# Kernel tuning notes

Measured on AMD Instinct MI355X. Metric: run time of the kernel, lower is better.

Reference implementation:

```python
import jax, jax.numpy as jnp
import numpy as np

N = 100000   # nodes
F = 128      # feature dim (== numEdges ctor arg)
H = 64       # hidden_dim
E = 1600000  # edges (avg degree 16)


def setup_inputs() -> dict:
    key = jax.random.key(0)
    ks = jax.random.split(key, 8)
    x = jax.random.normal(ks[0], (N, F), dtype=jnp.float32)
    edge_index = jax.random.randint(ks[1], (2, E), 0, N)
    sF = 1.0 / np.sqrt(F)
    sH = 1.0 / np.sqrt(H)
    conv_W = jax.random.normal(ks[2], (F, F), dtype=jnp.float32) * sF  # GCNConv linear weight
    conv_b = jnp.zeros((F,), dtype=jnp.float32)
    w1 = jax.random.normal(ks[3], (H, F), dtype=jnp.float32) * sF
    b1 = jnp.zeros((H,), dtype=jnp.float32)
    w2 = jax.random.normal(ks[4], (H, H), dtype=jnp.float32) * sH
    b2 = jnp.zeros((H,), dtype=jnp.float32)
    w3 = jax.random.normal(ks[5], (1, H), dtype=jnp.float32) * sH
    b3 = jnp.zeros((1,), dtype=jnp.float32)
    return dict(x=x, edge_index=edge_index, conv_W=conv_W, conv_b=conv_b,
                w1=w1, b1=b1, w2=w2, b2=b2, w3=w3, b3=b3)


def reference(x, edge_index, conv_W, conv_b, w1, b1, w2, b2, w3, b3):
    n = x.shape[0]
    # --- GCNConv: D^{-1/2}(A+I)D^{-1/2} X W + b ---
    xw = x @ conv_W.T                                   # [N, F]
    loops = jnp.arange(n)
    src = jnp.concatenate([edge_index[0], loops])       # add self-loops
    dst = jnp.concatenate([edge_index[1], loops])
    deg = jax.ops.segment_sum(jnp.ones(src.shape[0], xw.dtype), dst, num_segments=n)
    dinv = jnp.where(deg > 0, jax.lax.rsqrt(deg), 0.0)
    norm = dinv[src] * dinv[dst]                        # [E+N]
    h = jax.ops.segment_sum(xw[src] * norm[:, None], dst, num_segments=n) + conv_b  # [N, F]
    # --- MedianAggregation (index=None -> single segment, 'lower' interpolation) ---
    med = jnp.sort(h, axis=0)[(n - 1) // 2][None, :]    # [1, F]
    # --- tanh MLP ---
    a = jnp.tanh(med @ w1.T + b1)
    a = jnp.tanh(a @ w2.T + b2)
    return a @ w3.T + b3                                # [1, 1]
```

## Files before the change

### kernel.cpp

```cpp
#include <hip/hip_runtime.h>
#include <math.h>


#define CAP    24576
#define CCAP   96
#define CSTR   97
#define DSTR   32
#define OVCAP  4096
#define SPCAP  2048
#define BCAP   4608
#define NBKMAX 400
#define CH     4096

typedef __attribute__((ext_vector_type(8))) short short8;
typedef __attribute__((ext_vector_type(4))) float f32x4;
typedef __attribute__((ext_vector_type(8))) _Float16 half8;
typedef __attribute__((ext_vector_type(2))) _Float16 half2v;

__device__ __forceinline__ unsigned ordKey(float x) {
    unsigned u = __float_as_uint(x);
    return (u & 0x80000000u) ? ~u : (u | 0x80000000u);
}
__device__ __forceinline__ unsigned short f2bf(float f) {
    unsigned u = __float_as_uint(f);
    return (unsigned short)((u + 0x7FFFu + ((u >> 16) & 1u)) >> 16);
}

__global__ void k_init(int* __restrict__ cursor, int* __restrict__ below,
                       int* __restrict__ candCnt, int* __restrict__ ovCnt,
                       const float* __restrict__ W, short* __restrict__ Whi,
                       short* __restrict__ Wlo, int nbk) {
    if (blockIdx.x == 1) {
        for (int idx = threadIdx.x; idx < 16384; idx += 256) {
            int j = idx & 7, lane = (idx >> 3) & 63;
            int t = (idx >> 9) & 7, s = idx >> 12;
            int row = t * 16 + (lane & 15);
            int k = s * 32 + (lane >> 4) * 8 + j;
            float w = W[row * 128 + k];
            unsigned short hb = f2bf(w);
            float hf = __uint_as_float((unsigned)hb << 16);
            Whi[idx] = (short)hb;
            Wlo[idx] = (short)f2bf(w - hf);
        }
        return;
    }
    int t = threadIdx.x;
    for (int i = t; i < nbk; i += 256) cursor[i] = 0;
    if (t < 128) { below[t] = 0; candCnt[t] = 0; }
    if (t == 0) { ovCnt[0] = 0; ovCnt[1] = 0; ovCnt[2] = 0; }
}

__global__ __launch_bounds__(256) void k_gemm(
        const float* __restrict__ x, const short* __restrict__ Whi,
        const short* __restrict__ Wlo, _Float16* __restrict__ xw, int n) {
    __shared__ float trn[4 * 16 * 132];
    const int t = threadIdx.x;
    const int lane = t & 63, wv = t >> 6;
    const int quad = lane >> 4, m = lane & 15;
    const int rowBase = blockIdx.x * 64 + wv * 16;
    const int r = rowBase + m;
    const int rl = r < n ? r : (n - 1);
    f32x4 acc[8];
    #pragma unroll
    for (int q = 0; q < 8; q++) acc[q] = (f32x4){0.f, 0.f, 0.f, 0.f};
    #pragma unroll
    for (int s = 0; s < 4; s++) {
        const float* xp = x + (size_t)rl * 128 + s * 32 + quad * 8;
        float4 p0 = *(const float4*)xp;
        float4 p1 = *(const float4*)(xp + 4);
        float f[8] = {p0.x, p0.y, p0.z, p0.w, p1.x, p1.y, p1.z, p1.w};
        short8 ah, al;
        #pragma unroll
        for (int j = 0; j < 8; j++) {
            unsigned short hb = f2bf(f[j]);
            float hf = __uint_as_float((unsigned)hb << 16);
            ah[j] = (short)hb;
            al[j] = (short)f2bf(f[j] - hf);
        }
        #pragma unroll
        for (int q = 0; q < 8; q++) {
            short8 bh = *(const short8*)(Whi + (((s * 8 + q) * 64 + lane) << 3));
            short8 bl = *(const short8*)(Wlo + (((s * 8 + q) * 64 + lane) << 3));
            acc[q] = __builtin_amdgcn_mfma_f32_16x16x32_bf16(ah, bh, acc[q], 0, 0, 0);
            acc[q] = __builtin_amdgcn_mfma_f32_16x16x32_bf16(al, bh, acc[q], 0, 0, 0);
            acc[q] = __builtin_amdgcn_mfma_f32_16x16x32_bf16(ah, bl, acc[q], 0, 0, 0);
        }
    }
    float* tw = trn + wv * (16 * 132);
    #pragma unroll
    for (int q = 0; q < 8; q++)
        #pragma unroll
        for (int e = 0; e < 4; e++)
            tw[(quad * 4 + e) * 132 + q * 16 + m] = acc[q][e];
    #pragma unroll
    for (int i = 0; i < 4; i++) {
        int row = i * 4 + (lane >> 4);
        int c8 = lane & 15;
        const float* tp = tw + row * 132 + c8 * 8;
        float4 p0 = *(const float4*)tp;
        float4 p1 = *(const float4*)(tp + 4);
        half8 o;
        o[0] = (_Float16)p0.x; o[1] = (_Float16)p0.y;
        o[2] = (_Float16)p0.z; o[3] = (_Float16)p0.w;
        o[4] = (_Float16)p1.x; o[5] = (_Float16)p1.y;
        o[6] = (_Float16)p1.z; o[7] = (_Float16)p1.w;
        int grow = rowBase + row;
        if (grow < n) *(half8*)(xw + (size_t)grow * 128 + c8 * 8) = o;
    }
}

__global__ __launch_bounds__(256) void k_bin(
        const int* __restrict__ src, const int* __restrict__ dst, int E,
        int* __restrict__ cursor, int2* __restrict__ binned,
        int* __restrict__ ovCnt, int2* __restrict__ ovBuf, int nbk) {
    __shared__ char smem[39168];
    const int t = threadIdx.x;
    int2* stage = (int2*)smem;
    int* hist  = (int*)(smem + 32768);
    int* gbase = hist + NBKMAX;
    int* hist2 = gbase + NBKMAX;
    int* sbase = hist2 + NBKMAX;
    const int e0 = (int)blockIdx.x * CH;
    const int len = min(CH, E - e0);
    for (int i = t; i < nbk; i += 256) { hist[i] = 0; hist2[i] = 0; }
    __syncthreads();
    for (int k = t; k < len; k += 256) {
        int s = src[e0 + k], d = dst[e0 + k];
        stage[k] = make_int2(s, d);
        atomicAdd(&hist[d >> 8], 1);
    }
    __syncthreads();
    for (int i = t; i < nbk; i += 256) {
        int c = hist[i];
        if (c) {
            int g = atomicAdd(&cursor[i], c);
            if (g + c <= BCAP) gbase[i] = g;
            else {
                gbase[i] = -1;
                sbase[i] = atomicAdd(ovCnt, c);
            }
        }
    }
    __syncthreads();
    for (int k = t; k < len; k += 256) {
        int2 e = stage[k];
        int b = e.y >> 8;
        int p = atomicAdd(&hist2[b], 1);
        int g = gbase[b];
        if (g >= 0) binned[(size_t)b * BCAP + g + p] = e;
        else {
            int o = sbase[b] + p;
            if (o < OVCAP) ovBuf[o] = make_int2(e.y, e.x);
        }
    }
}

__global__ __launch_bounds__(512) void k_build(int2* __restrict__ binned,
                                               const int* __restrict__ cursor,
                                               float* __restrict__ dinv,
                                               unsigned char* __restrict__ deg8,
                                               int* __restrict__ ovCnt,
                                               int2* __restrict__ ovBuf,
                                               int* __restrict__ spillNodes, int n) {
    __shared__ int ladj[256 * DSTR];
    __shared__ int lcnt[256];
    const int b = blockIdx.x, t = threadIdx.x;
    const int cnt = min(cursor[b], BCAP);
    const size_t e0 = (size_t)b * BCAP;
    if (t < 256) lcnt[t] = 0;
    __syncthreads();
    for (int k = t; k < cnt; k += 512) {
        int2 e = binned[e0 + k];
        int li = e.y & 255;
        int pos = atomicAdd(&lcnt[li], 1);
        if (pos < DSTR) ladj[li * DSTR + pos] = e.x;
        else {
            int o = atomicAdd(ovCnt, 1);
            if (o < OVCAP) ovBuf[o] = make_int2(e.y, e.x);
        }
    }
    __syncthreads();
    int4* adjOut = (int4*)((int*)binned + e0 * 2);
    const int4* lsrc4 = (const int4*)ladj;
    for (int i = t; i < 2048; i += 512) adjOut[i] = lsrc4[i];
    if (t < 256) {
        int node = b * 256 + t;
        if (node < n) {
            int deg = lcnt[t];
            dinv[node] = (float)(1.0 / sqrt((double)(deg + 1)));
            deg8[node] = (unsigned char)(deg < 255 ? deg : 255);
            if (deg > DSTR) {
                int p = atomicAdd(ovCnt + 1, 1);
                if (p < SPCAP) spillNodes[p] = node;
            }
        }
    }
}

__global__ __launch_bounds__(256) void k_aggH(const _Float16* __restrict__ xw,
                                              const unsigned char* __restrict__ deg8,
                                              const int* __restrict__ adjAll,
                                              const float* __restrict__ dinv,
                                              const float* __restrict__ conv_b,
                                              _Float16* __restrict__ h,
                                              int n0, int n1) {
    const int d = n0 + blockIdx.x * 4 + (threadIdx.x >> 6);
    if (d >= n1) return;
    const int lane = threadIdx.x & 63;
    const int l32 = lane & 31;
    int degT = deg8[d];
    const int degB = degT < DSTR ? degT : DSTR;
    const float dd = dinv[d];
    const int* adjRow = adjAll + (size_t)(d >> 8) * (BCAP * 2) + (d & 255) * DSTR;
    int aj = adjRow[l32];
    bool ev = (lane < 32) && (l32 < degB);
    int ajs = ev ? aj : 0;
    float dv = ev ? dinv[ajs] : 0.f;
    const half2v* xwv = (const half2v*)xw;
    half2v a = xwv[(size_t)d * 64 + lane];
    float ax = dd * dd * (float)a.x, ay = dd * dd * (float)a.y;
    int j = 0;
    for (; j + 8 <= degB; j += 8) {
        int s[8];
        float w[8];
        #pragma unroll
        for (int q = 0; q < 8; q++) {
            s[q] = __shfl(ajs, j + q, 64);
            w[q] = dd * __shfl(dv, j + q, 64);
        }
        #pragma unroll
        for (int q = 0; q < 8; q++) {
            half2v v = xwv[(size_t)s[q] * 64 + lane];
            ax += w[q] * (float)v.x;
            ay += w[q] * (float)v.y;
        }
    }
    if (j < degB) {
        int s[8];
        float w[8];
        #pragma unroll
        for (int q = 0; q < 8; q++) {
            int idx = j + q;
            bool ok = idx < degB;
            int lsrc = ok ? idx : 0;
            int sv = __shfl(ajs, lsrc, 64);
            float wv = dd * __shfl(dv, lsrc, 64);
            s[q] = ok ? sv : 0;
            w[q] = ok ? wv : 0.f;
        }
        #pragma unroll
        for (int q = 0; q < 8; q++) {
            half2v v = xwv[(size_t)s[q] * 64 + lane];
            ax += w[q] * (float)v.x;
            ay += w[q] * (float)v.y;
        }
    }
    float2 cb = ((const float2*)conv_b)[lane];
    half2v o;
    o.x = (_Float16)(ax + cb.x);
    o.y = (_Float16)(ay + cb.y);
    ((half2v*)h)[(size_t)d * 64 + lane] = o;
}

__global__ __launch_bounds__(256) void k_sampleSpill(
        _Float16* h, int n,
        unsigned* __restrict__ Lkey, unsigned* __restrict__ Ukey,
        const _Float16* __restrict__ xw, const int* __restrict__ spillNodes,
        const int* __restrict__ adjAll, const float* __restrict__ dinv,
        const float* __restrict__ conv_b, const int2* __restrict__ ovBuf,
        const int* __restrict__ ovCnt) {
    const int t = threadIdx.x;
    if (blockIdx.x >= 128) {
        int m = ovCnt[0];  if (m > OVCAP) m = OVCAP;
        int sp = ovCnt[1]; if (sp > SPCAP) sp = SPCAP;
        if (t >= 128) return;
        for (int i = (int)blockIdx.x - 128; i < sp; i += 16) {
            const int d = spillNodes[i];
            const float dd = dinv[d];
            float acc = dd * dd * (float)xw[(size_t)d * 128 + t];
            const int* adjRow = adjAll + (size_t)(d >> 8) * (BCAP * 2) + (d & 255) * DSTR;
            for (int j = 0; j < DSTR; j++) {
                int a = adjRow[j];
                acc += dd * dinv[a] * (float)xw[(size_t)a * 128 + t];
            }
            for (int k = 0; k < m; k++) {
                int2 e = ovBuf[k];
                if (e.x == d)
                    acc += dd * dinv[e.y] * (float)xw[(size_t)e.y * 128 + t];
            }
            h[(size_t)d * 128 + t] = (_Float16)(acc + conv_b[t]);
        }
        return;
    }
    __shared__ int hist[2048];
    __shared__ int wsum[4];
    const int c = blockIdx.x;
    for (int i = t; i < 2048; i += 256) hist[i] = 0;
    __syncthreads();
    const int ns = (n + 31) >> 5;
    for (int i = t; i < ns; i += 256) {
        float v = (float)h[(size_t)(i << 5) * 128 + c];
        atomicAdd(&hist[ordKey(v) >> 21], 1);
    }
    __syncthreads();
    int ps = 0;
    #pragma unroll
    for (int b = 0; b < 8; b++) ps += hist[t * 8 + b];
    const int lane = t & 63, wv = t >> 6;
    int sc = ps;
    #pragma unroll
    for (int off = 1; off < 64; off <<= 1) {
        int y = __shfl_up(sc, off, 64);
        if (lane >= off) sc += y;
    }
    if (lane == 63) wsum[wv] = sc;
    __syncthreads();
    int wbase = 0;
    for (int ww = 0; ww < wv; ww++) wbase += wsum[ww];
    const int excl = wbase + sc - ps;
    const int sMid = (ns - 1) >> 1;
    const int delta = (int)(4.0f * sqrtf((float)ns)) + 1;
    int sLo = sMid - delta; if (sLo < 0) sLo = 0;
    int sHi = sMid + delta; if (sHi > ns - 1) sHi = ns - 1;
    if (sLo >= excl && sLo < excl + ps) {
        int rem = sLo - excl, b = t * 8;
        for (;; b++) { int cc = hist[b]; if (rem < cc) break; rem -= cc; }
        Lkey[c] = (unsigned)b << 21;
    }
    if (sHi >= excl && sHi < excl + ps) {
        int rem = sHi - excl, b = t * 8;
        for (;; b++) { int cc = hist[b]; if (rem < cc) break; rem -= cc; }
        Ukey[c] = (((unsigned)(b + 1)) << 21) - 1u;
    }
}

__global__ __launch_bounds__(256) void k_classify(const _Float16* __restrict__ h,
                                                  int total8,
                                                  const unsigned* __restrict__ Lkey,
                                                  const unsigned* __restrict__ Ukey,
                                                  int* __restrict__ below,
                                                  int* __restrict__ candCnt,
                                                  _Float16* __restrict__ cand) {
    __shared__ _Float16 buf[128 * CSTR];
    __shared__ int cN[128], cB[128];
    const int t = threadIdx.x;
    for (int i = t; i < 128; i += 256) { cN[i] = 0; cB[i] = 0; }
    __syncthreads();
    const int stride = gridDim.x * blockDim.x;
    const int i0 = blockIdx.x * blockDim.x + t;
    const int jb = (i0 << 3) & 127;
    unsigned L[8], U[8];
    #pragma unroll
    for (int k = 0; k < 8; k++) { L[k] = Lkey[jb + k]; U[k] = Ukey[jb + k]; }
    int b[8] = {0, 0, 0, 0, 0, 0, 0, 0};
    const half8* hv = (const half8*)h;
    for (int i = i0; i < total8; i += stride) {
        half8 v = hv[i];
        #pragma unroll
        for (int k = 0; k < 8; k++) {
            float f = (float)v[k];
            unsigned u = ordKey(f);
            if (u < L[k]) b[k]++;
            else if (u <= U[k]) {
                int p = atomicAdd(&cN[jb + k], 1);
                if (p < CCAP) buf[(jb + k) * CSTR + p] = v[k];
                else {
                    int g = atomicAdd(&candCnt[jb + k], 1);
                    if (g < CAP) cand[(size_t)(jb + k) * CAP + g] = v[k];
                }
            }
        }
    }
    #pragma unroll
    for (int k = 0; k < 8; k++)
        if (b[k]) atomicAdd(&cB[jb + k], b[k]);
    __syncthreads();
    if (t < 128) {
        if (cB[t]) atomicAdd(&below[t], cB[t]);
        int nn = cN[t] < CCAP ? cN[t] : CCAP;
        if (nn) {
            int base = atomicAdd(&candCnt[t], nn);
            for (int k2 = 0; k2 < nn && base + k2 < CAP; k2++)
                cand[(size_t)t * CAP + base + k2] = buf[t * CSTR + k2];
        }
    }
}

__global__ __launch_bounds__(256) void k_finalMlp(
        const _Float16* __restrict__ cand, const int* __restrict__ candCnt,
        const int* __restrict__ below, int n, float* __restrict__ med,
        int* __restrict__ doneCnt,
        const float* __restrict__ w1, const float* __restrict__ b1,
        const float* __restrict__ w2, const float* __restrict__ b2,
        const float* __restrict__ w3, const float* __restrict__ b3,
        float* __restrict__ out) {
    __shared__ int hist[2048];
    __shared__ int sSel;
    __shared__ int sRank;
    __shared__ int lastFlag;
    const int c = blockIdx.x, t = threadIdx.x;
    int cnt = candCnt[c]; if (cnt > CAP) cnt = CAP;
    const unsigned short* cp = (const unsigned short*)(cand + (size_t)c * CAP);
    if (t == 0) {
        int r = (n - 1) / 2 - below[c];
        if (r < 0) r = 0;
        if (r >= cnt) r = cnt - 1;
        sRank = r;
        sSel = 0;
    }
    for (int i = t; i < 2048; i += 256) hist[i] = 0;
    __syncthreads();
    for (int i = t; i < cnt; i += 256) {
        unsigned ub = cp[i];
        unsigned k = (ub & 0x8000u) ? (~ub & 0xFFFFu) : (ub | 0x8000u);
        atomicAdd(&hist[k >> 5], 1);
    }
    __syncthreads();
    if (t < 64) {
        int ps = 0;
        for (int b = t * 32; b < t * 32 + 32; b++) ps += hist[b];
        int sc = ps;
        #pragma unroll
        for (int off = 1; off < 64; off <<= 1) {
            int y = __shfl_up(sc, off, 64);
            if (t >= off) sc += y;
        }
        int excl = sc - ps;
        int r = sRank;
        if (excl <= r && r < sc) {
            int b = t * 32, rem = r - excl;
            for (;; b++) {
                int cc = hist[b];
                if (rem < cc) break;
                rem -= cc;
            }
            sSel = b;
            sRank = rem;
        }
    }
    __syncthreads();
    if (t < 32) hist[t] = 0;
    __syncthreads();
    const int sel = sSel;
    for (int i = t; i < cnt; i += 256) {
        unsigned ub = cp[i];
        unsigned k = (ub & 0x8000u) ? (~ub & 0xFFFFu) : (ub | 0x8000u);
        if ((int)(k >> 5) == sel) atomicAdd(&hist[k & 31], 1);
    }
    __syncthreads();
    if (t == 0) {
        int rem = sRank, b = 0;
        for (;; b++) {
            int cc = hist[b];
            if (rem < cc) break;
            rem -= cc;
        }
        unsigned key16 = ((unsigned)sel << 5) | (unsigned)b;
        unsigned short bits = (key16 & 0x8000u) ? (unsigned short)(key16 & 0x7FFFu)
                                                : (unsigned short)(~key16 & 0xFFFFu);
        _Float16 hv;
        *(unsigned short*)&hv = bits;
        med[c] = (float)hv;
        __threadfence();
        int old = atomicAdd(doneCnt, 1);
        lastFlag = (old == 127);
    }
    __syncthreads();
    if (!lastFlag) return;
    __threadfence();
    __shared__ float m[128], a1[64], a2[64];
    if (t < 128) m[t] = med[t];
    __syncthreads();
    if (t < 64) {
        float acc = b1[t];
        for (int f = 0; f < 128; f++) acc += m[f] * w1[t * 128 + f];
        a1[t] = tanhf(acc);
    }
    __syncthreads();
    if (t < 64) {
        float acc = b2[t];
        for (int f = 0; f < 64; f++) acc += a1[f] * w2[t * 64 + f];
        a2[t] = tanhf(acc);
    }
    __syncthreads();
    if (t == 0) {
        float acc = b3[0];
        for (int f = 0; f < 64; f++) acc += a2[f] * w3[f];
        out[0] = acc;
    }
}

extern "C" void kernel_launch(void* const* d_in, const int* in_sizes, int n_in,
                              void* d_out, int out_size, void* d_ws, size_t ws_size,
                              hipStream_t stream) {
    const float* x      = (const float*)d_in[0];
    const int*   ei     = (const int*)d_in[1];
    const float* conv_W = (const float*)d_in[2];
    const float* conv_b = (const float*)d_in[3];
    const float* w1 = (const float*)d_in[4];
    const float* b1 = (const float*)d_in[5];
    const float* w2 = (const float*)d_in[6];
    const float* b2 = (const float*)d_in[7];
    const float* w3 = (const float*)d_in[8];
    const float* b3 = (const float*)d_in[9];

    const int N = in_sizes[0] / 128;
    const int E = in_sizes[1] / 2;
    const int* src = ei;
    const int* dst = ei + E;
    const int NBK = (N + 255) / 256;

    char* p = (char*)d_ws;
    auto alloc = [&](size_t bytes) -> char* {
        char* q = p;
        p += (bytes + 255) & ~(size_t)255;
        return q;
    };
    _Float16* xw  = (_Float16*)alloc((size_t)N * 128 * 2);
    _Float16* h   = (_Float16*)alloc((size_t)N * 128 * 2);
    int2*  binned = (int2*)alloc((size_t)NBK * BCAP * 8);
    _Float16* cand = (_Float16*)alloc((size_t)128 * CAP * 2);
    float* dinv   = (float*)alloc((size_t)N * 4);
    unsigned char* deg8 = (unsigned char*)alloc((size_t)N);
    int*   cursor = (int*)alloc((size_t)NBK * 4);
    short* Whi    = (short*)alloc(16384 * 2);
    short* Wlo    = (short*)alloc(16384 * 2);
    int2*  ovBuf  = (int2*)alloc((size_t)OVCAP * 8);
    int*   ovCnt  = (int*)alloc(256);
    int*   spillNodes = (int*)alloc((size_t)SPCAP * 4);
    unsigned* Lkey = (unsigned*)alloc(128 * 4);
    unsigned* Ukey = (unsigned*)alloc(128 * 4);
    int*   below   = (int*)alloc(128 * 4);
    int*   candCnt = (int*)alloc(128 * 4);
    float* med     = (float*)alloc(128 * 4);

    const int GB   = (N + 63) / 64;
    const int BINB = (E + CH - 1) / CH;
    const int NH   = ((N / 2) + 3) & ~3;

    k_init<<<2, 256, 0, stream>>>(cursor, below, candCnt, ovCnt, conv_W, Whi, Wlo, NBK);
    k_gemm<<<GB, 256, 0, stream>>>(x, Whi, Wlo, xw, N);
    k_bin<<<BINB, 256, 0, stream>>>(src, dst, E, cursor, binned, ovCnt, ovBuf, NBK);
    k_build<<<NBK, 512, 0, stream>>>(binned, cursor, dinv, deg8, ovCnt, ovBuf,
                                     spillNodes, N);
    k_aggH<<<(NH + 3) / 4, 256, 0, stream>>>(xw, deg8, (const int*)binned, dinv,
                                             conv_b, h, 0, NH);
    k_aggH<<<(N - NH + 3) / 4, 256, 0, stream>>>(xw, deg8, (const int*)binned, dinv,
                                                 conv_b, h, NH, N);
    k_sampleSpill<<<144, 256, 0, stream>>>(h, N, Lkey, Ukey, xw, spillNodes,
                                           (const int*)binned, dinv, conv_b,
                                           ovBuf, ovCnt);
    k_classify<<<512, 256, 0, stream>>>(h, N * 16, Lkey, Ukey, below, candCnt, cand);
    k_finalMlp<<<128, 256, 0, stream>>>(cand, candCnt, below, N, med, ovCnt + 2,
                                        w1, b1, w2, b2, w3, b3, (float*)d_out);
}
```

Measured before the change: 308.9 us.

## Replace histogram median selection with register-resident bitwise radix search

The final selection kernel no longer builds two shared-memory histograms with atomics. Each thread loads up to 96 fp16 keys into registers, and the block runs a 16-step bitwise binary search on the key value, counting keys below each pivot with wave reductions and a shared-memory sum. This removes LDS atomic contention and the serial scan over bins. In exchange it does 16 passes over the register array with two barriers per step, and the 96-entry register array may spill.

```diff
diff --git a/kernel.cpp b/kernel.cpp
--- a/kernel.cpp
+++ b/kernel.cpp
@@ -3,6 +3,7 @@
 
 
 #define CAP    24576
+#define MPT    96
 #define CCAP   96
 #define CSTR   97
 #define DSTR   32
@@ -394,70 +395,40 @@
         const float* __restrict__ w2, const float* __restrict__ b2,
         const float* __restrict__ w3, const float* __restrict__ b3,
         float* __restrict__ out) {
-    __shared__ int hist[2048];
-    __shared__ int sSel;
-    __shared__ int sRank;
+    __shared__ int wsum[4];
     __shared__ int lastFlag;
     const int c = blockIdx.x, t = threadIdx.x;
+    const int lane = t & 63, wv = t >> 6;
     int cnt = candCnt[c]; if (cnt > CAP) cnt = CAP;
-    const unsigned short* cp = (const unsigned short*)(cand + (size_t)c * CAP);
+    const unsigned short* cp = (const unsigned short*)cand + (size_t)c * CAP;
+    int r = (n - 1) / 2 - below[c];
+    if (r < 0) r = 0;
+    if (r >= cnt) r = cnt - 1;
+    unsigned short myk[MPT];
+    #pragma unroll
+    for (int mi = 0; mi < MPT; mi++) {
+        int i = t + mi * 256;
+        unsigned ub = (i < cnt) ? (unsigned)cp[i] : 0u;
+        unsigned k = (ub & 0x8000u) ? (~ub & 0xFFFFu) : (ub | 0x8000u);
+        myk[mi] = (i < cnt) ? (unsigned short)k : (unsigned short)0xFFFFu;
+    }
+    unsigned cur = 0;
+    for (int bit = 15; bit >= 0; bit--) {
+        const unsigned pivot = cur | (1u << bit);
+        int lc = 0;
+        #pragma unroll
+        for (int mi = 0; mi < MPT; mi++) lc += ((unsigned)myk[mi] < pivot) ? 1 : 0;
+        #pragma unroll
+        for (int off = 32; off > 0; off >>= 1) lc += __shfl_down(lc, off, 64);
+        if (lane == 0) wsum[wv] = lc;
+        __syncthreads();
+        int tot = wsum[0] + wsum[1] + wsum[2] + wsum[3];
+        if (tot <= r) cur = pivot;
+        __syncthreads();
+    }
     if (t == 0) {
-        int r = (n - 1) / 2 - below[c];
-        if (r < 0) r = 0;
-        if (r >= cnt) r = cnt - 1;
-        sRank = r;
-        sSel = 0;
-    }
-    for (int i = t; i < 2048; i += 256) hist[i] = 0;
-    __syncthreads();
-    for (int i = t; i < cnt; i += 256) {
-        unsigned ub = cp[i];
-        unsigned k = (ub & 0x8000u) ? (~ub & 0xFFFFu) : (ub | 0x8000u);
-        atomicAdd(&hist[k >> 5], 1);
-    }
-    __syncthreads();
-    if (t < 64) {
-        int ps = 0;
-        for (int b = t * 32; b < t * 32 + 32; b++) ps += hist[b];
-        int sc = ps;
-        #pragma unroll
-        for (int off = 1; off < 64; off <<= 1) {
-            int y = __shfl_up(sc, off, 64);
-            if (t >= off) sc += y;
-        }
-        int excl = sc - ps;
-        int r = sRank;
-        if (excl <= r && r < sc) {
-            int b = t * 32, rem = r - excl;
-            for (;; b++) {
-                int cc = hist[b];
-                if (rem < cc) break;
-                rem -= cc;
-            }
-            sSel = b;
-            sRank = rem;
-        }
-    }
-    __syncthreads();
-    if (t < 32) hist[t] = 0;
-    __syncthreads();
-    const int sel = sSel;
-    for (int i = t; i < cnt; i += 256) {
-        unsigned ub = cp[i];
-        unsigned k = (ub & 0x8000u) ? (~ub & 0xFFFFu) : (ub | 0x8000u);
-        if ((int)(k >> 5) == sel) atomicAdd(&hist[k & 31], 1);
-    }
-    __syncthreads();
-    if (t == 0) {
-        int rem = sRank, b = 0;
-        for (;; b++) {
-            int cc = hist[b];
-            if (rem < cc) break;
-            rem -= cc;
-        }
-        unsigned key16 = ((unsigned)sel << 5) | (unsigned)b;
-        unsigned short bits = (key16 & 0x8000u) ? (unsigned short)(key16 & 0x7FFFu)
-                                                : (unsigned short)(~key16 & 0xFFFFu);
+        unsigned short bits = (cur & 0x8000u) ? (unsigned short)(cur & 0x7FFFu)
+                                              : (unsigned short)(~cur & 0xFFFFu);
         _Float16 hv;
         *(unsigned short*)&hv = bits;
         med[c] = (float)hv;
```

Result: no change. 310.7 us (+0.6%).
